# Performance work log

Hardware: AMD Instinct MI355X
Metric: run time of the kernel (lower is better)

Reference implementation:

```python
import jax, jax.numpy as jnp
import numpy as np

H = 128        # hidden_size
VOCAB = 1000   # per-cat-type vocab (len(fn_mapping[t]))
NCAT_T = 4     # number of categorical node types
NCONT_T = 4    # number of continuous node types
N_CAT = 200_000
N_CONT = 150_000
N_TXN = 150_000
F_TXN = 371    # hard-coded transaction feature width in source


def setup_inputs() -> dict:
    key = jax.random.key(0)
    ks = jax.random.split(key, 10)
    return {
        "cat_tables": jax.random.normal(ks[0], (NCAT_T, VOCAB, H), dtype=jnp.float32),
        "cont_w": jax.random.normal(ks[1], (NCONT_T, H), dtype=jnp.float32),
        "cont_b": jax.random.normal(ks[2], (NCONT_T, H), dtype=jnp.float32),
        "txn_w": jax.random.normal(ks[3], (F_TXN, H), dtype=jnp.float32) * 0.05,
        "txn_b": jax.random.normal(ks[4], (H,), dtype=jnp.float32),
        "txn_feats": jax.random.normal(ks[5], (N_TXN, F_TXN), dtype=jnp.float32),
        "cont_values": jax.random.normal(ks[6], (N_CONT,), dtype=jnp.float32),
        "cat_type_ids": jax.random.randint(ks[7], (N_CAT,), 0, NCAT_T, dtype=jnp.int32),
        "cat_value_ids": jax.random.randint(ks[8], (N_CAT,), 0, VOCAB, dtype=jnp.int32),
        "cont_type_ids": jax.random.randint(ks[9], (N_CONT,), 0, NCONT_T, dtype=jnp.int32),
    }


def reference(cat_tables, cont_w, cont_b, txn_w, txn_b, txn_feats,
              cont_values, cat_type_ids, cat_value_ids, cont_type_ids):
    # Categorical path: Embedding lookup, batched over all cat nodes via
    # a fused (type, value) gather into the stacked per-type tables.
    cat_out = cat_tables[cat_type_ids, cat_value_ids]            # [N_CAT, H]
    # Continuous path: Linear(1, H) per node == value * w[type] + b[type].
    cont_out = cont_values[:, None] * cont_w[cont_type_ids] + cont_b[cont_type_ids]  # [N_CONT, H]
    # Transaction path: single GEMM replaces per-row Linear(371, H) calls.
    txn_out = txn_feats @ txn_w + txn_b                          # [N_TXN, H]
    # Original returns a Python list in node order; batched form is the
    # concatenation over the type-partitioned node groups.
    return jnp.concatenate([cat_out, cont_out, txn_out], axis=0)  # [N, H]
```

## Files before the change

kernel.cpp:

```cpp
#include <hip/hip_runtime.h>

#define HID    128
#define VOCAB  1000
#define N_CAT  200000
#define N_CONT 150000
#define N_TXN  150000
#define F_TXN  371
#define NSTEP  12
#define OUT_TXN_BASE (N_CAT + N_CONT)

#define SLAB_ROWS   16
#define SLAB_F32    (SLAB_ROWS * F_TXN)
#define SLAB_CHUNKS (SLAB_F32 / 4)
#define LROW        392
#define SLAB_SHORTS (SLAB_ROWS * LROW)
#define NSLAB       (N_TXN / SLAB_ROWS)
#define PBLK        512
#define CLSLAB(x)   ((x) < NSLAB ? (x) : (NSLAB - 1))

typedef __attribute__((ext_vector_type(4))) float f32x4;
typedef __attribute__((ext_vector_type(8))) short bf16x8;

__device__ __forceinline__ unsigned short f2bf(float x) {
    union { float f; unsigned u; } c; c.f = x;
    unsigned r = c.u + 0x7FFF + ((c.u >> 16) & 1);
    return (unsigned short)(r >> 16);
}

__device__ __forceinline__ unsigned cvt_pk(float lo, float hi) {
    unsigned r;
    asm("v_cvt_pk_bf16_f32 %0, %1, %2" : "=v"(r) : "v"(lo), "v"(hi));
    return r;
}

union BFrag { bf16x8 v; unsigned u[4]; };

#define CAT_BLOCKS  (N_CAT / 8)
#define CONT_BLOCKS (N_CONT / 8)
__global__ __launch_bounds__(256) void catcont_kernel(
    const float* __restrict__ tables, const int* __restrict__ tids, const int* __restrict__ vids,
    const float* __restrict__ w, const float* __restrict__ b,
    const float* __restrict__ vals, const int* __restrict__ ctids,
    float* __restrict__ out)
{
    int bid = blockIdx.x;
    if (bid < CAT_BLOCKS) {
        int tid = bid * 256 + threadIdx.x;
        int row = tid >> 5;
        int h   = (tid & 31) << 2;
        long src = ((long)tids[row] * VOCAB + vids[row]) * HID + h;
        f32x4 v = *reinterpret_cast<const f32x4*>(tables + src);
        __builtin_nontemporal_store(v, reinterpret_cast<f32x4*>(out + (long)row * HID + h));
    } else {
        int tid = (bid - CAT_BLOCKS) * 256 + threadIdx.x;
        int row = tid >> 5;
        int h   = (tid & 31) << 2;
        int t   = ctids[row];
        float v = vals[row];
        f32x4 wv = *reinterpret_cast<const f32x4*>(w + t * HID + h);
        f32x4 bv = *reinterpret_cast<const f32x4*>(b + t * HID + h);
        f32x4 r  = v * wv + bv;
        __builtin_nontemporal_store(r, reinterpret_cast<f32x4*>(out + (long)(N_CAT + row) * HID + h));
    }
}

__global__ __launch_bounds__(256) void txn_persist_kernel(
    const float* __restrict__ feats, const float* __restrict__ txn_w,
    const float* __restrict__ bias, float* __restrict__ out)
{
    __shared__ __align__(16) unsigned short Alds[2 * SLAB_SHORTS];

    const int t    = threadIdx.x;
    const int lane = t & 63;
    const int w    = t >> 6;
    const int r16  = lane & 15;
    const int kg   = lane >> 4;

    BFrag Bf0[NSTEP], Bf1[NSTEP];
    const int c0 = w * 32 + r16, c1 = c0 + 16;
    const float bv0 = bias[c0], bv1 = bias[c1];
    #pragma unroll
    for (int s = 0; s < NSTEP; ++s) {
        #pragma unroll
        for (int h = 0; h < 4; ++h) {
            int k = s * 32 + kg * 8 + h * 2;
            float w0 = (k     < F_TXN) ? txn_w[(long)k * HID + c0]       : 0.f;
            float w1 = (k + 1 < F_TXN) ? txn_w[(long)(k + 1) * HID + c0] : 0.f;
            Bf0[s].u[h] = cvt_pk(w0, w1);
            float x0 = (k     < F_TXN) ? txn_w[(long)k * HID + c1]       : 0.f;
            float x1 = (k + 1 < F_TXN) ? txn_w[(long)(k + 1) * HID + c1] : 0.f;
            Bf1[s].u[h] = cvt_pk(x0, x1);
        }
    }

    bool sval[6];
    unsigned wa0[6], wa1[6];
    #pragma unroll
    for (int i = 0; i < 6; ++i) {
        int q = i * 256 + t;
        sval[i] = (q < SLAB_CHUNKS);
        int qq = sval[i] ? q : 0;
        unsigned a[4];
        #pragma unroll
        for (int j = 0; j < 4; ++j) {
            int e   = qq * 4 + j;
            int r   = e / F_TXN;
            int col = e - r * F_TXN;
            a[j] = (unsigned)(r * LROW + col);
        }
        wa0[i] = a[0] | (a[1] << 16);
        wa1[i] = a[2] | (a[3] << 16);
    }

    for (int z = t; z < 2 * SLAB_ROWS * 13; z += 256) {
        int b  = z / (SLAB_ROWS * 13);
        int rm = z - b * (SLAB_ROWS * 13);
        int r  = rm / 13;
        int cc = rm - r * 13;
        Alds[b * SLAB_SHORTS + r * LROW + F_TXN + cc] = 0;
    }

    f32x4 arA[6], arB[6];

    auto gload = [&](f32x4 (&ar)[6], int sl) {
        size_t S0 = (size_t)sl * SLAB_F32;
        #pragma unroll
        for (int i = 0; i < 6; ++i)
            if (sval[i])
                ar[i] = *reinterpret_cast<const f32x4*>(feats + S0 + (size_t)(i * 256 + t) * 4);
    };
    auto swrite = [&](int buf, const f32x4 (&ar)[6]) {
        unsigned short* dst = Alds + buf * SLAB_SHORTS;
        #pragma unroll
        for (int i = 0; i < 6; ++i)
            if (sval[i]) {
                unsigned lo = cvt_pk(ar[i][0], ar[i][1]);
                unsigned hi = cvt_pk(ar[i][2], ar[i][3]);
                dst[wa0[i] & 0xffffu] = (unsigned short)lo;
                dst[wa0[i] >> 16]     = (unsigned short)(lo >> 16);
                dst[wa1[i] & 0xffffu] = (unsigned short)hi;
                dst[wa1[i] >> 16]     = (unsigned short)(hi >> 16);
            }
    };

    const int bid = blockIdx.x;
    int sl  = bid;
    int cur = 0;

    gload(arA, sl);
    swrite(0, arA);
    gload(arA, CLSLAB(sl + PBLK));
    __syncthreads();

    auto iter = [&](const f32x4 (&pend)[6], f32x4 (&tgt)[6]) {
        gload(tgt, CLSLAB(sl + 2 * PBLK));
        __builtin_amdgcn_sched_barrier(0);

        f32x4 acc0 = f32x4{0.f, 0.f, 0.f, 0.f};
        f32x4 acc1 = f32x4{0.f, 0.f, 0.f, 0.f};
        const unsigned short* Ar = Alds + cur * SLAB_SHORTS + r16 * LROW;
        #pragma unroll
        for (int s = 0; s < NSTEP; ++s) {
            bf16x8 af = *reinterpret_cast<const bf16x8*>(Ar + s * 32 + kg * 8);
            acc0 = __builtin_amdgcn_mfma_f32_16x16x32_bf16(af, Bf0[s].v, acc0, 0, 0, 0);
            acc1 = __builtin_amdgcn_mfma_f32_16x16x32_bf16(af, Bf1[s].v, acc1, 0, 0, 0);
        }

        swrite(cur ^ 1, pend);

        long R0 = (long)sl * SLAB_ROWS + kg * 4;
        #pragma unroll
        for (int j = 0; j < 4; ++j) {
            float* o = out + (OUT_TXN_BASE + R0 + j) * HID;
            __builtin_nontemporal_store(acc0[j] + bv0, o + c0);
            __builtin_nontemporal_store(acc1[j] + bv1, o + c0 + 16);
        }

        asm volatile("s_waitcnt lgkmcnt(0)" ::: "memory");
        __builtin_amdgcn_s_barrier();
        __builtin_amdgcn_sched_barrier(0);
        cur ^= 1;
        sl  += PBLK;
    };

    while (sl < NSLAB) {
        iter(arA, arB);
        if (sl >= NSLAB) break;
        iter(arB, arA);
    }
}

extern "C" void kernel_launch(void* const* d_in, const int* in_sizes, int n_in,
                              void* d_out, int out_size, void* d_ws, size_t ws_size,
                              hipStream_t stream) {
    const float* cat_tables    = (const float*)d_in[0];
    const float* cont_w        = (const float*)d_in[1];
    const float* cont_b        = (const float*)d_in[2];
    const float* txn_w         = (const float*)d_in[3];
    const float* txn_b         = (const float*)d_in[4];
    const float* txn_feats     = (const float*)d_in[5];
    const float* cont_values   = (const float*)d_in[6];
    const int*   cat_type_ids  = (const int*)d_in[7];
    const int*   cat_value_ids = (const int*)d_in[8];
    const int*   cont_type_ids = (const int*)d_in[9];
    float* out = (float*)d_out;

    txn_persist_kernel<<<PBLK, 256, 0, stream>>>(txn_feats, txn_w, txn_b, out);
    catcont_kernel<<<CAT_BLOCKS + CONT_BLOCKS, 256, 0, stream>>>(
        cat_tables, cat_type_ids, cat_value_ids,
        cont_w, cont_b, cont_values, cont_type_ids, out);
}
```

Before: 84.36 us.

## Double slab rows to 32 and prefetch one slab ahead in txn GEMM

Grows each slab in the persistent transaction GEMM from 16 to 32 rows. Each wave now issues four MFMAs per K step and reuses its register-resident weight fragments across two row tiles. The register prefetch drops from two slabs ahead to one, with a single 12-entry register array, and bounds guards handle a partial last slab. This gives more bytes in flight per load batch and fewer loop iterations. The cost is more registers and LDS per block and a shallower prefetch depth that may expose more global load latency.

```diff
diff --git a/kernel.cpp b/kernel.cpp
--- a/kernel.cpp
+++ b/kernel.cpp
@@ -9,23 +9,17 @@
 #define NSTEP  12
 #define OUT_TXN_BASE (N_CAT + N_CONT)
 
-#define SLAB_ROWS   16
+#define SLAB_ROWS   32
 #define SLAB_F32    (SLAB_ROWS * F_TXN)
 #define SLAB_CHUNKS (SLAB_F32 / 4)
 #define LROW        392
 #define SLAB_SHORTS (SLAB_ROWS * LROW)
-#define NSLAB       (N_TXN / SLAB_ROWS)
+#define NSLAB       ((N_TXN + SLAB_ROWS - 1) / SLAB_ROWS)
+#define A_ELEMS     ((size_t)N_TXN * F_TXN)
 #define PBLK        512
-#define CLSLAB(x)   ((x) < NSLAB ? (x) : (NSLAB - 1))
 
 typedef __attribute__((ext_vector_type(4))) float f32x4;
 typedef __attribute__((ext_vector_type(8))) short bf16x8;
-
-__device__ __forceinline__ unsigned short f2bf(float x) {
-    union { float f; unsigned u; } c; c.f = x;
-    unsigned r = c.u + 0x7FFF + ((c.u >> 16) & 1);
-    return (unsigned short)(r >> 16);
-}
 
 __device__ __forceinline__ unsigned cvt_pk(float lo, float hi) {
     unsigned r;
@@ -93,10 +87,10 @@
         }
     }
 
-    bool sval[6];
-    unsigned wa0[6], wa1[6];
+    bool sval[12];
+    unsigned wa0[12], wa1[12];
     #pragma unroll
-    for (int i = 0; i < 6; ++i) {
+    for (int i = 0; i < 12; ++i) {
         int q = i * 256 + t;
         sval[i] = (q < SLAB_CHUNKS);
         int qq = sval[i] ? q : 0;
@@ -120,19 +114,22 @@
         Alds[b * SLAB_SHORTS + r * LROW + F_TXN + cc] = 0;
     }
 
-    f32x4 arA[6], arB[6];
-
-    auto gload = [&](f32x4 (&ar)[6], int sl) {
+    f32x4 ar[12];
+
+    auto gload = [&](int sl) {
         size_t S0 = (size_t)sl * SLAB_F32;
         #pragma unroll
-        for (int i = 0; i < 6; ++i)
-            if (sval[i])
-                ar[i] = *reinterpret_cast<const f32x4*>(feats + S0 + (size_t)(i * 256 + t) * 4);
+        for (int i = 0; i < 12; ++i)
+            if (sval[i]) {
+                size_t ge = S0 + (size_t)(i * 256 + t) * 4;
+                if (ge > A_ELEMS - 4) ge = A_ELEMS - 4;
+                ar[i] = *reinterpret_cast<const f32x4*>(feats + ge);
+            }
     };
-    auto swrite = [&](int buf, const f32x4 (&ar)[6]) {
+    auto swrite = [&](int buf) {
         unsigned short* dst = Alds + buf * SLAB_SHORTS;
         #pragma unroll
-        for (int i = 0; i < 6; ++i)
+        for (int i = 0; i < 12; ++i)
             if (sval[i]) {
                 unsigned lo = cvt_pk(ar[i][0], ar[i][1]);
                 unsigned hi = cvt_pk(ar[i][2], ar[i][3]);
@@ -144,49 +141,54 @@
     };
 
     const int bid = blockIdx.x;
-    int sl  = bid;
+    gload(bid);
+    swrite(0);
+    __syncthreads();
+
     int cur = 0;
-
-    gload(arA, sl);
-    swrite(0, arA);
-    gload(arA, CLSLAB(sl + PBLK));
-    __syncthreads();
-
-    auto iter = [&](const f32x4 (&pend)[6], f32x4 (&tgt)[6]) {
-        gload(tgt, CLSLAB(sl + 2 * PBLK));
+    #pragma unroll 1
+    for (int sl = bid; sl < NSLAB; sl += PBLK) {
+        int  nxt      = sl + PBLK;
+        bool have_nxt = (nxt < NSLAB);
+        if (have_nxt) gload(nxt);
         __builtin_amdgcn_sched_barrier(0);
 
-        f32x4 acc0 = f32x4{0.f, 0.f, 0.f, 0.f};
-        f32x4 acc1 = f32x4{0.f, 0.f, 0.f, 0.f};
-        const unsigned short* Ar = Alds + cur * SLAB_SHORTS + r16 * LROW;
+        f32x4 acc00 = f32x4{0.f,0.f,0.f,0.f}, acc01 = f32x4{0.f,0.f,0.f,0.f};
+        f32x4 acc10 = f32x4{0.f,0.f,0.f,0.f}, acc11 = f32x4{0.f,0.f,0.f,0.f};
+        const unsigned short* Ar0 = Alds + cur * SLAB_SHORTS + r16 * LROW;
+        const unsigned short* Ar1 = Ar0 + 16 * LROW;
         #pragma unroll
         for (int s = 0; s < NSTEP; ++s) {
-            bf16x8 af = *reinterpret_cast<const bf16x8*>(Ar + s * 32 + kg * 8);
-            acc0 = __builtin_amdgcn_mfma_f32_16x16x32_bf16(af, Bf0[s].v, acc0, 0, 0, 0);
-            acc1 = __builtin_amdgcn_mfma_f32_16x16x32_bf16(af, Bf1[s].v, acc1, 0, 0, 0);
-        }
-
-        swrite(cur ^ 1, pend);
+            bf16x8 af0 = *reinterpret_cast<const bf16x8*>(Ar0 + s * 32 + kg * 8);
+            bf16x8 af1 = *reinterpret_cast<const bf16x8*>(Ar1 + s * 32 + kg * 8);
+            acc00 = __builtin_amdgcn_mfma_f32_16x16x32_bf16(af0, Bf0[s].v, acc00, 0, 0, 0);
+            acc01 = __builtin_amdgcn_mfma_f32_16x16x32_bf16(af0, Bf1[s].v, acc01, 0, 0, 0);
+            acc10 = __builtin_amdgcn_mfma_f32_16x16x32_bf16(af1, Bf0[s].v, acc10, 0, 0, 0);
+            acc11 = __builtin_amdgcn_mfma_f32_16x16x32_bf16(af1, Bf1[s].v, acc11, 0, 0, 0);
+        }
+
+        if (have_nxt) swrite(cur ^ 1);
 
         long R0 = (long)sl * SLAB_ROWS + kg * 4;
         #pragma unroll
         for (int j = 0; j < 4; ++j) {
-            float* o = out + (OUT_TXN_BASE + R0 + j) * HID;
-            __builtin_nontemporal_store(acc0[j] + bv0, o + c0);
-            __builtin_nontemporal_store(acc1[j] + bv1, o + c0 + 16);
+            long r0 = R0 + j, r1 = R0 + 16 + j;
+            if (r0 < N_TXN) {
+                float* o = out + (OUT_TXN_BASE + r0) * HID;
+                __builtin_nontemporal_store(acc00[j] + bv0, o + c0);
+                __builtin_nontemporal_store(acc01[j] + bv1, o + c0 + 16);
+            }
+            if (r1 < N_TXN) {
+                float* o = out + (OUT_TXN_BASE + r1) * HID;
+                __builtin_nontemporal_store(acc10[j] + bv0, o + c0);
+                __builtin_nontemporal_store(acc11[j] + bv1, o + c0 + 16);
+            }
         }
 
         asm volatile("s_waitcnt lgkmcnt(0)" ::: "memory");
         __builtin_amdgcn_s_barrier();
         __builtin_amdgcn_sched_barrier(0);
         cur ^= 1;
-        sl  += PBLK;
-    };
-
-    while (sl < NSLAB) {
-        iter(arA, arB);
-        if (sl >= NSLAB) break;
-        iter(arB, arA);
     }
 }
 
```

Measured after the change: 83.60 us. Within noise of the previous version (-0.9%).
